# Optimization experiments

Hardware: AMD Instinct MI355X
Metric: run time of the kernel (lower is better)

The kernel has to match this reference:

```python
import jax, jax.numpy as jnp
import numpy as np

D = 1024
M = 32768
B = 4096
TEMP = 1.0
LN_EPS = 1e-5


def setup_inputs() -> dict:
    key = jax.random.key(0)
    ks = jax.random.split(key, 8)
    s = 1.0 / np.sqrt(D)
    return {
        "query": jax.random.normal(ks[0], (B, D), dtype=jnp.float32),
        "mem": jax.random.normal(ks[1], (M, D), dtype=jnp.float32),
        "Wq": jax.random.normal(ks[2], (D, D), dtype=jnp.float32) * s,
        "bq": jax.random.normal(ks[3], (D,), dtype=jnp.float32) * 0.01,
        "Wk": jax.random.normal(ks[4], (D, D), dtype=jnp.float32) * s,
        "bk": jax.random.normal(ks[5], (D,), dtype=jnp.float32) * 0.01,
        "Wv": jax.random.normal(ks[6], (D, D), dtype=jnp.float32) * s,
        "bv": jax.random.normal(ks[7], (D,), dtype=jnp.float32) * 0.01,
        "gamma": jnp.ones((D,), dtype=jnp.float32),
        "beta": jnp.zeros((D,), dtype=jnp.float32),
        "k": 8,
    }


def reference(query, mem, Wq, bq, Wk, bk, Wv, bv, gamma, beta, k):
    d = query.shape[-1]
    # Linear projections (torch Linear: x @ W.T + b)
    q = query @ Wq.T + bq            # [B, d]
    K = mem @ Wk.T + bk              # [M, d]
    V = mem @ Wv.T + bv              # [M, d]
    # Scaled similarity matrix
    sims = (q @ K.T) / (jnp.sqrt(jnp.asarray(d, q.dtype)) * TEMP)  # [B, M]
    # Top-k selection, then irregular gather of V rows
    _, topi = jax.lax.top_k(sims, k)  # [B, k]
    ret = V[topi]                     # [B, k, d]
    # LayerNorm over last dim (elementwise affine, eps=1e-5, biased var)
    mu = jnp.mean(ret, axis=-1, keepdims=True)
    var = jnp.var(ret, axis=-1, keepdims=True)
    return (ret - mu) * jax.lax.rsqrt(var + LN_EPS) * gamma + beta
```

## Files before the change

kernel.cpp:

```cpp
#include <hip/hip_runtime.h>
#include <hip/hip_bf16.h>
#include <math.h>

#define D_DIM 1024
#define B_ROWS 4096
#define M_ROWS 32768
#define TOPK 8
#define TOPC 16
#define TOPB 8
#define NCB (M_ROWS / 128)

typedef __attribute__((ext_vector_type(8))) short bf16x8;
typedef __attribute__((ext_vector_type(4))) float f32x4;

__device__ __forceinline__ unsigned short f32_to_bf16(float f) {
  unsigned int u = __float_as_uint(f);
  unsigned int r = (u + 0x7FFFu + ((u >> 16) & 1u)) >> 16;
  return (unsigned short)r;
}
__device__ __forceinline__ float bf16_to_f32(unsigned short h) {
  return __uint_as_float(((unsigned int)h) << 16);
}
__device__ __forceinline__ void async_copy16(void* lds, const void* g) {
  __builtin_amdgcn_global_load_lds(
      (const __attribute__((address_space(1))) unsigned int*)g,
      (__attribute__((address_space(3))) unsigned int*)lds, 16, 0, 0);
}

template <int N>
__device__ __forceinline__ void insN(float v, int idx,
                                     float* __restrict__ tv,
                                     int* __restrict__ ti) {
  if (v < tv[N - 1]) return;
  if (v == tv[N - 1] && idx > ti[N - 1]) return;
  float cv = v;
  int ci = idx;
#pragma unroll
  for (int p = 0; p < N; ++p) {
    if (cv > tv[p] || (cv == tv[p] && ci < ti[p])) {
      const float t0 = tv[p]; tv[p] = cv; cv = t0;
      const int t1 = ti[p]; ti[p] = ci; ci = t1;
    }
  }
}

__global__ __launch_bounds__(256) void gram_f64(
    const float* __restrict__ Wq, const float* __restrict__ Wk,
    double* __restrict__ G)
{
  __shared__ float sA[2][32][68];
  __shared__ float sB[2][32][68];
  const int tid = threadIdx.x;
  const int tx = tid & 15, ty = tid >> 4;
  const int f0 = blockIdx.x * 64;
  const int e0 = blockIdx.y * 64;

  double acc[4][4];
#pragma unroll
  for (int i = 0; i < 4; ++i)
#pragma unroll
    for (int j = 0; j < 4; ++j) acc[i][j] = 0.0;

  auto STAGE = [&](int d, int k0) {
#pragma unroll
    for (int it = 0; it < 2; ++it) {
      const int L = it * 256 + tid;
      const int kk = L >> 4, c4 = (L & 15) * 4;
      *(float4*)&sA[d][kk][c4] = *(const float4*)(Wq + (size_t)(k0 + kk) * D_DIM + f0 + c4);
      *(float4*)&sB[d][kk][c4] = *(const float4*)(Wk + (size_t)(k0 + kk) * D_DIM + e0 + c4);
    }
  };

  STAGE(0, 0);
  __syncthreads();
  int cur = 0;
  for (int t = 0; t < 32; ++t) {
    if (t < 31) STAGE(cur ^ 1, (t + 1) * 32);
#pragma unroll
    for (int kk = 0; kk < 32; ++kk) {
      const double a[4] = {sA[cur][kk][ty * 4 + 0], sA[cur][kk][ty * 4 + 1],
                           sA[cur][kk][ty * 4 + 2], sA[cur][kk][ty * 4 + 3]};
      const double b[4] = {sB[cur][kk][tx * 4 + 0], sB[cur][kk][tx * 4 + 1],
                           sB[cur][kk][tx * 4 + 2], sB[cur][kk][tx * 4 + 3]};
#pragma unroll
      for (int i = 0; i < 4; ++i)
#pragma unroll
        for (int j = 0; j < 4; ++j)
          acc[i][j] = fma(a[i], b[j], acc[i][j]);
    }
    __syncthreads();
    cur ^= 1;
  }
#pragma unroll
  for (int i = 0; i < 4; ++i)
#pragma unroll
    for (int j = 0; j < 4; ++j)
      G[(size_t)(f0 + ty * 4 + i) * D_DIM + e0 + tx * 4 + j] = acc[i][j];
}

__global__ __launch_bounds__(256) void bias_terms(
    const float* __restrict__ Wq, const float* __restrict__ Wk,
    const float* __restrict__ bq, const float* __restrict__ bk,
    double* __restrict__ wvec, double* __restrict__ ubias,
    double* __restrict__ s0)
{
  const int blk = blockIdx.x;
  const int tid = threadIdx.x;
  if (blk < 4) {
    const int c = blk * 256 + tid;
    double acc = 0.0;
    for (int n = 0; n < D_DIM; ++n)
      acc = fma((double)Wq[(size_t)n * D_DIM + c], (double)bk[n], acc);
    wvec[c] = acc;
  } else if (blk < 8) {
    const int c = (blk - 4) * 256 + tid;
    double acc = 0.0;
    for (int n = 0; n < D_DIM; ++n)
      acc = fma((double)Wk[(size_t)n * D_DIM + c], (double)bq[n], acc);
    ubias[c] = acc;
  } else {
    double acc = 0.0;
#pragma unroll
    for (int i = 0; i < 4; ++i) {
      const int idx = tid * 4 + i;
      acc = fma((double)bq[idx], (double)bk[idx], acc);
    }
#pragma unroll
    for (int off = 32; off > 0; off >>= 1) acc += __shfl_down(acc, off);
    __shared__ double red[4];
    if ((tid & 63) == 0) red[tid >> 6] = acc;
    __syncthreads();
    if (tid == 0) s0[0] = red[0] + red[1] + red[2] + red[3];
  }
}

__global__ __launch_bounds__(256) void qbk_w(
    const float* __restrict__ query, const double* __restrict__ w,
    const double* __restrict__ s0, double* __restrict__ qbk)
{
  const int b = blockIdx.x * 4 + (threadIdx.x >> 6);
  const int lane = threadIdx.x & 63;
  const float* qrow = query + (size_t)b * D_DIM + lane * 16;
  const double* wrow = w + lane * 16;
  double acc = 0.0;
#pragma unroll
  for (int i = 0; i < 16; ++i)
    acc = fma((double)qrow[i], wrow[i], acc);
#pragma unroll
  for (int off = 32; off > 0; off >>= 1) acc += __shfl_down(acc, off);
  if (lane == 0) qbk[b] = acc + s0[0];
}

__global__ __launch_bounds__(256) void uproj_G(
    const float* __restrict__ query, const double* __restrict__ G,
    const double* __restrict__ ubias, double* __restrict__ U)
{
  __shared__ double sAdT[2][32][66];
  __shared__ double sBd[2][32][68];
  const int tid = threadIdx.x;
  const int tx = tid & 15, ty = tid >> 4;
  const int row0 = blockIdx.x * 64;
  const int col0 = blockIdx.y * 64;

  double acc[4][4];
#pragma unroll
  for (int i = 0; i < 4; ++i)
#pragma unroll
    for (int j = 0; j < 4; ++j) acc[i][j] = 0.0;

  auto STAGE = [&](int d, int k0) {
#pragma unroll
    for (int it = 0; it < 2; ++it) {
      const int L = it * 256 + tid;
      const int rowa = L >> 3, c4 = (L & 7) * 4;
      const float4 v =
          *(const float4*)(query + (size_t)(row0 + rowa) * D_DIM + k0 + c4);
      sAdT[d][c4 + 0][rowa] = (double)v.x;
      sAdT[d][c4 + 1][rowa] = (double)v.y;
      sAdT[d][c4 + 2][rowa] = (double)v.z;
      sAdT[d][c4 + 3][rowa] = (double)v.w;
    }
#pragma unroll
    for (int it = 0; it < 4; ++it) {
      const int L = it * 256 + tid;
      const int kk = L >> 5, c2 = (L & 31) * 2;
      *(double2*)&sBd[d][kk][c2] =
          *(const double2*)(G + (size_t)(k0 + kk) * D_DIM + col0 + c2);
    }
  };

  STAGE(0, 0);
  __syncthreads();
  int cur = 0;
  for (int t = 0; t < 32; ++t) {
    if (t < 31) STAGE(cur ^ 1, (t + 1) * 32);
#pragma unroll
    for (int kk = 0; kk < 32; ++kk) {
      const double2 p0 = *(const double2*)&sAdT[cur][kk][ty * 4];
      const double2 p1 = *(const double2*)&sAdT[cur][kk][ty * 4 + 2];
      const double a[4] = {p0.x, p0.y, p1.x, p1.y};
      const double bb[4] = {sBd[cur][kk][tx * 4 + 0], sBd[cur][kk][tx * 4 + 1],
                            sBd[cur][kk][tx * 4 + 2], sBd[cur][kk][tx * 4 + 3]};
#pragma unroll
      for (int i = 0; i < 4; ++i)
#pragma unroll
        for (int j = 0; j < 4; ++j)
          acc[i][j] = fma(a[i], bb[j], acc[i][j]);
    }
    __syncthreads();
    cur ^= 1;
  }
  const double ub[4] = {ubias[col0 + tx * 4 + 0], ubias[col0 + tx * 4 + 1],
                        ubias[col0 + tx * 4 + 2], ubias[col0 + tx * 4 + 3]};
#pragma unroll
  for (int i = 0; i < 4; ++i) {
    const size_t base = (size_t)(row0 + ty * 4 + i) * D_DIM + col0 + tx * 4;
    *(double2*)(U + base)     = (double2){acc[i][0] + ub[0], acc[i][1] + ub[1]};
    *(double2*)(U + base + 2) = (double2){acc[i][2] + ub[2], acc[i][3] + ub[3]};
  }
}

#define SBUF3 12288
__global__ __launch_bounds__(512, 4) void sims_topc_gemm(
    const unsigned short* __restrict__ A, const unsigned short* __restrict__ B,
    float* __restrict__ part_v, int* __restrict__ part_i)
{
  __shared__ unsigned short smem[3 * SBUF3];

  const int tid = threadIdx.x;
  const int lane = tid & 63;
  const int wave = tid >> 6;
  const int wr = wave >> 1;
  const int wc = wave & 1;

  const int bid = blockIdx.x;
  const int x = bid & 7;
  const int t9 = bid >> 3;
  const int cbg = t9 >> 7;
  const int r = (t9 >> 3) & 15;
  const int cbl = t9 & 7;
  const int cb = (x * 4 + cbg) * 8 + cbl;
  const int row0 = r * 256;
  const int col0 = cb * 128;

  const int st_r = lane >> 2;
  const int st_swz = ((lane & 3) ^ ((st_r >> 1) & 3)) * 16;

  auto STAGE = [&](int d, int k0) {
    unsigned short* buf = smem + d * SBUF3;
#pragma unroll
    for (int i = 0; i < 3; ++i) {
      const int seg = wave * 3 + i;
      if (seg < 16) {
        const int grow = row0 + seg * 16 + st_r;
        async_copy16((char*)(buf + seg * 512),
                     (const char*)(A + (size_t)grow * D_DIM + k0) + st_swz);
      } else {
        const int s2 = seg - 16;
        const int grow = col0 + s2 * 16 + st_r;
        async_copy16((char*)(buf + 8192 + s2 * 512),
                     (const char*)(B + (size_t)grow * D_DIM + k0) + st_swz);
      }
    }
  };

  f32x4 acc[4][4];
#pragma unroll
  for (int m = 0; m < 4; ++m)
#pragma unroll
    for (int n = 0; n < 4; ++n) acc[m][n] = (f32x4){0.f, 0.f, 0.f, 0.f};

  auto COMPUTE = [&](int d) {
    const unsigned short* sA = smem + d * SBUF3;
    const unsigned short* sB = sA + 8192;
    bf16x8 af[4], bfr[4];
    const int ch = lane >> 4;
#pragma unroll
    for (int m = 0; m < 4; ++m) {
      const int Ra = wr * 64 + m * 16 + (lane & 15);
      af[m] = *(const bf16x8*)((const char*)sA + Ra * 64 + ((ch ^ ((Ra >> 1) & 3)) * 16));
    }
#pragma unroll
    for (int n = 0; n < 4; ++n) {
      const int Rb = wc * 64 + n * 16 + (lane & 15);
      bfr[n] = *(const bf16x8*)((const char*)sB + Rb * 64 + ((ch ^ ((Rb >> 1) & 3)) * 16));
    }
    __builtin_amdgcn_s_setprio(1);
#pragma unroll
    for (int m = 0; m < 4; ++m)
#pragma unroll
      for (int n = 0; n < 4; ++n)
        acc[m][n] = __builtin_amdgcn_mfma_f32_16x16x32_bf16(af[m], bfr[n], acc[m][n], 0, 0, 0);
    __builtin_amdgcn_s_setprio(0);
  };

  STAGE(0, 0);
  STAGE(1, 32);
  asm volatile("s_waitcnt vmcnt(3)" ::: "memory");
  __builtin_amdgcn_sched_barrier(0);
  __builtin_amdgcn_s_barrier();

  for (int tt = 0; tt < 30; tt += 3) {
    STAGE(2, (tt + 2) * 32);
    COMPUTE(0);
    asm volatile("s_waitcnt vmcnt(3)" ::: "memory");
    __builtin_amdgcn_sched_barrier(0);
    __builtin_amdgcn_s_barrier();

    STAGE(0, (tt + 3) * 32);
    COMPUTE(1);
    asm volatile("s_waitcnt vmcnt(3)" ::: "memory");
    __builtin_amdgcn_sched_barrier(0);
    __builtin_amdgcn_s_barrier();

    STAGE(1, (tt + 4) * 32);
    COMPUTE(2);
    asm volatile("s_waitcnt vmcnt(3)" ::: "memory");
    __builtin_amdgcn_sched_barrier(0);
    __builtin_amdgcn_s_barrier();
  }
  COMPUTE(0);
  asm volatile("s_waitcnt vmcnt(0)" ::: "memory");
  __builtin_amdgcn_sched_barrier(0);
  __builtin_amdgcn_s_barrier();
  COMPUTE(1);
  __builtin_amdgcn_sched_barrier(0);
  __builtin_amdgcn_s_barrier();

#pragma unroll
  for (int m = 0; m < 4; ++m)
#pragma unroll
    for (int n = 0; n < 4; ++n)
#pragma unroll
      for (int rg = 0; rg < 4; ++rg) {
        const int row = wr * 64 + m * 16 + (lane >> 4) * 4 + rg;
        const int colL = wc * 64 + n * 16 + (lane & 15);
        smem[row * 132 + colL] = f32_to_bf16(acc[m][n][rg]);
      }
  __syncthreads();

  {
    const int row = tid & 255;
    const int h = tid >> 8;
    float tv[4];
    int ti_[4];
#pragma unroll
    for (int p = 0; p < 4; ++p) { tv[p] = -INFINITY; ti_[p] = 0; }
    const unsigned short* crow = smem + row * 132 + h * 64;
    const int gcol = col0 + h * 64;
    for (int j = 0; j < 64; j += 4) {
      const ushort4 c4 = *(const ushort4*)(crow + j);
      insN<4>(bf16_to_f32(c4.x), gcol + j + 0, tv, ti_);
      insN<4>(bf16_to_f32(c4.y), gcol + j + 1, tv, ti_);
      insN<4>(bf16_to_f32(c4.z), gcol + j + 2, tv, ti_);
      insN<4>(bf16_to_f32(c4.w), gcol + j + 3, tv, ti_);
    }
    const size_t base = ((size_t)(row0 + row) * NCB + cb) * TOPB + h * 4;
    *(float4*)(part_v + base) = (float4){tv[0], tv[1], tv[2], tv[3]};
    *(int4*)(part_i + base)   = (int4){ti_[0], ti_[1], ti_[2], ti_[3]};
  }
}

__global__ __launch_bounds__(512, 4) void proj256_bf16(
    const unsigned short* __restrict__ A,
    const unsigned short* __restrict__ B,
    const float* __restrict__ bias,
    unsigned short* __restrict__ C)
{
  __shared__ unsigned short smem[3 * SBUF3];

  const int tid = threadIdx.x;
  const int lane = tid & 63;
  const int wave = tid >> 6;
  const int wr = wave >> 1;
  const int wc = wave & 1;

  const int row0 = blockIdx.x * 256;
  const int col0 = blockIdx.y * 128;

  const int st_r = lane >> 2;
  const int st_swz = ((lane & 3) ^ ((st_r >> 1) & 3)) * 16;

  auto STAGE = [&](int d, int k0) {
    unsigned short* buf = smem + d * SBUF3;
#pragma unroll
    for (int i = 0; i < 3; ++i) {
      const int seg = wave * 3 + i;
      if (seg < 16) {
        const int grow = row0 + seg * 16 + st_r;
        async_copy16((char*)(buf + seg * 512),
                     (const char*)(A + (size_t)grow * D_DIM + k0) + st_swz);
      } else {
        const int s2 = seg - 16;
        const int grow = col0 + s2 * 16 + st_r;
        async_copy16((char*)(buf + 8192 + s2 * 512),
                     (const char*)(B + (size_t)grow * D_DIM + k0) + st_swz);
      }
    }
  };

  f32x4 acc[4][4];
#pragma unroll
  for (int m = 0; m < 4; ++m)
#pragma unroll
    for (int n = 0; n < 4; ++n) acc[m][n] = (f32x4){0.f, 0.f, 0.f, 0.f};

  auto COMPUTE = [&](int d) {
    const unsigned short* sA = smem + d * SBUF3;
    const unsigned short* sB = sA + 8192;
    bf16x8 af[4], bfr[4];
    const int ch = lane >> 4;
#pragma unroll
    for (int m = 0; m < 4; ++m) {
      const int Ra = wr * 64 + m * 16 + (lane & 15);
      af[m] = *(const bf16x8*)((const char*)sA + Ra * 64 + ((ch ^ ((Ra >> 1) & 3)) * 16));
    }
#pragma unroll
    for (int n = 0; n < 4; ++n) {
      const int Rb = wc * 64 + n * 16 + (lane & 15);
      bfr[n] = *(const bf16x8*)((const char*)sB + Rb * 64 + ((ch ^ ((Rb >> 1) & 3)) * 16));
    }
    __builtin_amdgcn_s_setprio(1);
#pragma unroll
    for (int m = 0; m < 4; ++m)
#pragma unroll
      for (int n = 0; n < 4; ++n)
        acc[m][n] = __builtin_amdgcn_mfma_f32_16x16x32_bf16(af[m], bfr[n], acc[m][n], 0, 0, 0);
    __builtin_amdgcn_s_setprio(0);
  };

  STAGE(0, 0);
  STAGE(1, 32);
  asm volatile("s_waitcnt vmcnt(3)" ::: "memory");
  __builtin_amdgcn_sched_barrier(0);
  __builtin_amdgcn_s_barrier();

  for (int tt = 0; tt < 30; tt += 3) {
    STAGE(2, (tt + 2) * 32);
    COMPUTE(0);
    asm volatile("s_waitcnt vmcnt(3)" ::: "memory");
    __builtin_amdgcn_sched_barrier(0);
    __builtin_amdgcn_s_barrier();

    STAGE(0, (tt + 3) * 32);
    COMPUTE(1);
    asm volatile("s_waitcnt vmcnt(3)" ::: "memory");
    __builtin_amdgcn_sched_barrier(0);
    __builtin_amdgcn_s_barrier();

    STAGE(1, (tt + 4) * 32);
    COMPUTE(2);
    asm volatile("s_waitcnt vmcnt(3)" ::: "memory");
    __builtin_amdgcn_sched_barrier(0);
    __builtin_amdgcn_s_barrier();
  }
  COMPUTE(0);
  asm volatile("s_waitcnt vmcnt(0)" ::: "memory");
  __builtin_amdgcn_sched_barrier(0);
  __builtin_amdgcn_s_barrier();
  COMPUTE(1);

#pragma unroll
  for (int n = 0; n < 4; ++n) {
    const int col = col0 + wc * 64 + n * 16 + (lane & 15);
    const float bcol = bias[col];
#pragma unroll
    for (int m = 0; m < 4; ++m)
#pragma unroll
      for (int rg = 0; rg < 4; ++rg) {
        const int row = row0 + wr * 64 + m * 16 + (lane >> 4) * 4 + rg;
        C[(size_t)row * D_DIM + col] = f32_to_bf16(acc[m][n][rg] + bcol);
      }
  }
}

__global__ __launch_bounds__(256) void merge_rescore(
    const float* __restrict__ part_v, const int* __restrict__ part_i,
    const double* __restrict__ U, const double* __restrict__ qbk,
    const float* __restrict__ mem, int* __restrict__ topi)
{
  const int r = blockIdx.x;
  const int tid = threadIdx.x;
  const int lane = tid & 63;
  const int wave = tid >> 6;

  float tv[8];
  int ti[8];
  {
    const size_t base = ((size_t)r * NCB + tid) * TOPB;
    const float4 a0 = *(const float4*)(part_v + base);
    const float4 a1 = *(const float4*)(part_v + base + 4);
    const int4 b0 = *(const int4*)(part_i + base);
    const int4 b1 = *(const int4*)(part_i + base + 4);
    tv[0] = a0.x; tv[1] = a0.y; tv[2] = a0.z; tv[3] = a0.w;
    tv[4] = a1.x; tv[5] = a1.y; tv[6] = a1.z; tv[7] = a1.w;
    ti[0] = b0.x; ti[1] = b0.y; ti[2] = b0.z; ti[3] = b0.w;
    ti[4] = b1.x; ti[5] = b1.y; ti[6] = b1.z; ti[7] = b1.w;
  }
  unsigned rem = 0xFFu;

  __shared__ float wv4[4];
  __shared__ int wi4[4];
  __shared__ int winner;
  __shared__ int cand16[TOPC];

  for (int p = 0; p < TOPC; ++p) {
    float bv = -INFINITY;
    int bi = 0x7FFFFFFF;
#pragma unroll
    for (int e = 0; e < 8; ++e) {
      const bool alive = (rem >> e) & 1u;
      const float v = tv[e];
      const int ix = ti[e];
      if (alive && (v > bv || (v == bv && ix < bi))) { bv = v; bi = ix; }
    }
#pragma unroll
    for (int off = 32; off > 0; off >>= 1) {
      const float ov = __shfl_down(bv, off);
      const int oi = __shfl_down(bi, off);
      if (ov > bv || (ov == bv && oi < bi)) { bv = ov; bi = oi; }
    }
    if (lane == 0) { wv4[wave] = bv; wi4[wave] = bi; }
    __syncthreads();
    if (tid == 0) {
      float gv = wv4[0];
      int gi = wi4[0];
#pragma unroll
      for (int w = 1; w < 4; ++w)
        if (wv4[w] > gv || (wv4[w] == gv && wi4[w] < gi)) { gv = wv4[w]; gi = wi4[w]; }
      winner = gi;
      cand16[p] = gi;
    }
    __syncthreads();
    const int wgi = winner;
#pragma unroll
    for (int e = 0; e < 8; ++e)
      if (ti[e] == wgi) rem &= ~(1u << e);
  }

  __shared__ double sval[TOPC];
  __shared__ int sidx[TOPC];

  const double* urow = U + (size_t)r * D_DIM + lane * 16;
  double uv[16];
#pragma unroll
  for (int i = 0; i < 8; ++i) {
    const double2 d2 = *(const double2*)(urow + i * 2);
    uv[i * 2] = d2.x;
    uv[i * 2 + 1] = d2.y;
  }
  const double qb = qbk[r];

  for (int c = wave; c < TOPC; c += 4) {
    const int ci = cand16[c];
    const float* mrow = mem + (size_t)ci * D_DIM + lane * 16;
    double acc = 0.0;
#pragma unroll
    for (int i = 0; i < 4; ++i) {
      const float4 mv = *(const float4*)(mrow + i * 4);
      acc = fma(uv[i * 4 + 0], (double)mv.x, acc);
      acc = fma(uv[i * 4 + 1], (double)mv.y, acc);
      acc = fma(uv[i * 4 + 2], (double)mv.z, acc);
      acc = fma(uv[i * 4 + 3], (double)mv.w, acc);
    }
#pragma unroll
    for (int off = 32; off > 0; off >>= 1) acc += __shfl_down(acc, off);
    if (lane == 0) { sval[c] = acc + qb; sidx[c] = ci; }
  }
  __syncthreads();

  if (tid == 0) {
    bool used[TOPC];
#pragma unroll
    for (int p = 0; p < TOPC; ++p) used[p] = false;
#pragma unroll
    for (int p = 0; p < TOPK; ++p) {
      int best = -1;
      double bv = 0.0;
      int bi = 0;
      for (int c = 0; c < TOPC; ++c) {
        if (used[c]) continue;
        const double v = sval[c];
        const int ix = sidx[c];
        if (best < 0 || v > bv || (v == bv && ix < bi)) { best = c; bv = v; bi = ix; }
      }
      used[best] = true;
      topi[(size_t)r * TOPK + p] = bi;
    }
  }
}

#define N4_MEM   (M_ROWS * D_DIM / 4)
#define N4_QUERY (B_ROWS * D_DIM / 4)
#define N4_W     (D_DIM * D_DIM / 4)
#define N4_TOTAL (N4_MEM + N4_QUERY + 3 * N4_W)

__global__ __launch_bounds__(256) void cast_all_bf16(
    const float* __restrict__ mem, const float* __restrict__ query,
    const float* __restrict__ Wk, const float* __restrict__ Wv,
    const float* __restrict__ Wq,
    unsigned short* __restrict__ membf, unsigned short* __restrict__ querybf,
    unsigned short* __restrict__ wkbf, unsigned short* __restrict__ wvbf,
    unsigned short* __restrict__ wqbf)
{
  int i = blockIdx.x * 256 + threadIdx.x;
  if (i >= N4_TOTAL) return;
  const float* src;
  unsigned short* dst;
  if (i < N4_MEM) { src = mem; dst = membf; }
  else if ((i -= N4_MEM) < N4_QUERY) { src = query; dst = querybf; }
  else if ((i -= N4_QUERY) < N4_W) { src = Wk; dst = wkbf; }
  else if ((i -= N4_W) < N4_W) { src = Wv; dst = wvbf; }
  else { i -= N4_W; src = Wq; dst = wqbf; }
  const float4 v = *(const float4*)(src + (size_t)i * 4);
  ushort4 o;
  o.x = f32_to_bf16(v.x);
  o.y = f32_to_bf16(v.y);
  o.z = f32_to_bf16(v.z);
  o.w = f32_to_bf16(v.w);
  *(ushort4*)(dst + (size_t)i * 4) = o;
}

__global__ __launch_bounds__(256) void gather_ln(
    const unsigned short* __restrict__ V, const int* __restrict__ topi,
    const float* __restrict__ gamma, const float* __restrict__ beta,
    float* __restrict__ out)
{
  const int row = blockIdx.x;
  const int tid = threadIdx.x;
  const int idx = topi[row];
  const unsigned short* src = V + (size_t)idx * D_DIM;
  const ushort4 raw = *(const ushort4*)(src + tid * 4);
  const float v0 = bf16_to_f32(raw.x);
  const float v1 = bf16_to_f32(raw.y);
  const float v2 = bf16_to_f32(raw.z);
  const float v3 = bf16_to_f32(raw.w);
  float s = v0 + v1 + v2 + v3;
  float s2 = v0 * v0 + v1 * v1 + v2 * v2 + v3 * v3;
#pragma unroll
  for (int off = 32; off > 0; off >>= 1) {
    s += __shfl_down(s, off);
    s2 += __shfl_down(s2, off);
  }
  __shared__ float red[8];
  __shared__ float stats[2];
  const int wid = tid >> 6;
  if ((tid & 63) == 0) { red[wid] = s; red[4 + wid] = s2; }
  __syncthreads();
  if (tid == 0) {
    const float S = red[0] + red[1] + red[2] + red[3];
    const float S2 = red[4] + red[5] + red[6] + red[7];
    const float mu = S * (1.0f / D_DIM);
    const float var = S2 * (1.0f / D_DIM) - mu * mu;
    stats[0] = mu;
    stats[1] = rsqrtf(var + 1e-5f);
  }
  __syncthreads();
  const float mu = stats[0], rstd = stats[1];
  const float4 g4 = *(const float4*)(gamma + tid * 4);
  const float4 b4 = *(const float4*)(beta + tid * 4);
  float4 o;
  o.x = (v0 - mu) * rstd * g4.x + b4.x;
  o.y = (v1 - mu) * rstd * g4.y + b4.y;
  o.z = (v2 - mu) * rstd * g4.z + b4.z;
  o.w = (v3 - mu) * rstd * g4.w + b4.w;
  *(float4*)(out + (size_t)row * D_DIM + tid * 4) = o;
}

extern "C" void kernel_launch(void* const* d_in, const int* in_sizes, int n_in,
                              void* d_out, int out_size, void* d_ws, size_t ws_size,
                              hipStream_t stream)
{
  const float* query = (const float*)d_in[0];
  const float* mem   = (const float*)d_in[1];
  const float* Wq    = (const float*)d_in[2];
  const float* bq    = (const float*)d_in[3];
  const float* Wk    = (const float*)d_in[4];
  const float* bk    = (const float*)d_in[5];
  const float* Wv    = (const float*)d_in[6];
  const float* bv    = (const float*)d_in[7];
  const float* gamma = (const float*)d_in[8];
  const float* beta  = (const float*)d_in[9];
  float* out = (float*)d_out;

  char* ws = (char*)d_ws;
  double* u64 = (double*)ws;   ws += (size_t)B_ROWS * D_DIM * sizeof(double);
  double* G = (double*)ws;     ws += (size_t)D_DIM * D_DIM * sizeof(double);
  unsigned short* qbf = (unsigned short*)ws;
  ws += (size_t)B_ROWS * D_DIM * sizeof(unsigned short);
  unsigned short* querybf = (unsigned short*)ws;
  ws += (size_t)B_ROWS * D_DIM * sizeof(unsigned short);
  unsigned short* membf = (unsigned short*)ws;
  ws += (size_t)M_ROWS * D_DIM * sizeof(unsigned short);
  char* Aregion = ws;
  ws += (size_t)M_ROWS * D_DIM * sizeof(unsigned short)
      + 2 * (size_t)B_ROWS * NCB * TOPB * sizeof(float);
  double* wvec = (double*)ws;  ws += (size_t)D_DIM * sizeof(double);
  double* ubias = (double*)ws; ws += (size_t)D_DIM * sizeof(double);
  double* s0 = (double*)ws;    ws += 2 * sizeof(double);
  double* qbk = (double*)ws;   ws += (size_t)B_ROWS * sizeof(double);
  int* topi = (int*)ws;

  unsigned short* Kbf = (unsigned short*)Aregion;
  float* part_v = (float*)(Aregion + (size_t)M_ROWS * D_DIM * sizeof(unsigned short));
  int* part_i = (int*)((char*)part_v + (size_t)B_ROWS * NCB * TOPB * sizeof(float));
  unsigned short* wkbf = (unsigned short*)G;
  unsigned short* wvbf = wkbf + (size_t)D_DIM * D_DIM;
  unsigned short* wqbf = wvbf + (size_t)D_DIM * D_DIM;
  unsigned short* Vbf = (unsigned short*)Aregion;

  gram_f64<<<dim3(16, 16), 256, 0, stream>>>(Wq, Wk, G);
  bias_terms<<<dim3(9), 256, 0, stream>>>(Wq, Wk, bq, bk, wvec, ubias, s0);
  qbk_w<<<dim3(B_ROWS / 4), 256, 0, stream>>>(query, wvec, s0, qbk);
  uproj_G<<<dim3(B_ROWS / 64, D_DIM / 64), 256, 0, stream>>>(query, G, ubias, u64);

  cast_all_bf16<<<dim3((N4_TOTAL + 255) / 256), 256, 0, stream>>>(
      mem, query, Wk, Wv, Wq, membf, querybf, wkbf, wvbf, wqbf);

  proj256_bf16<<<dim3(M_ROWS / 256, D_DIM / 128), 512, 0, stream>>>(membf, wkbf, bk, Kbf);
  proj256_bf16<<<dim3(B_ROWS / 256, D_DIM / 128), 512, 0, stream>>>(querybf, wqbf, bq, qbf);

  sims_topc_gemm<<<dim3((B_ROWS / 256) * NCB), 512, 0, stream>>>(qbf, Kbf, part_v, part_i);
  merge_rescore<<<dim3(B_ROWS), 256, 0, stream>>>(part_v, part_i, u64, qbk, mem, topi);

  proj256_bf16<<<dim3(M_ROWS / 256, D_DIM / 128), 512, 0, stream>>>(membf, wvbf, bv, Vbf);
  gather_ln<<<dim3(B_ROWS * TOPK), 256, 0, stream>>>(Vbf, topi, gamma, beta, out);
}
```

Baseline: 1.154 ms.

## Fuse prep kernels, batch K/Q/V projections, pack top-k partials into u32

Merges the gram, bias, and bf16 cast kernels into one launch. The qbk dot product moves into merge_rescore. The three projection GEMMs become one grid, so K, Q and V are computed together, which needs separate workspace buffers for K and V. Per-tile top-4 partials are packed as bf16 value plus a 16-bit local index in one uint32, halving partial traffic. Partial values are now rounded to bf16, and querybf aliases the parts buffer, which relies on the ordering between kernels.

```diff
diff --git a/kernel.cpp b/kernel.cpp
--- a/kernel.cpp
+++ b/kernel.cpp
@@ -44,81 +44,87 @@
   }
 }
 
-__global__ __launch_bounds__(256) void gram_f64(
+#define N4_MEM   (M_ROWS * D_DIM / 4)
+#define N4_QUERY (B_ROWS * D_DIM / 4)
+#define N4_W     (D_DIM * D_DIM / 4)
+#define N4_TOTAL (N4_MEM + N4_QUERY + 3 * N4_W)
+#define NCAST_BLK ((N4_TOTAL + 255) / 256)
+
+__global__ __launch_bounds__(256) void gram_bias_cast(
     const float* __restrict__ Wq, const float* __restrict__ Wk,
-    double* __restrict__ G)
+    const float* __restrict__ bq, const float* __restrict__ bk,
+    const float* __restrict__ mem, const float* __restrict__ query,
+    const float* __restrict__ Wv,
+    double* __restrict__ G, double* __restrict__ wvec,
+    double* __restrict__ ubias, double* __restrict__ s0,
+    unsigned short* __restrict__ membf, unsigned short* __restrict__ querybf,
+    unsigned short* __restrict__ wkbf, unsigned short* __restrict__ wvbf,
+    unsigned short* __restrict__ wqbf)
 {
   __shared__ float sA[2][32][68];
   __shared__ float sB[2][32][68];
-  const int tid = threadIdx.x;
-  const int tx = tid & 15, ty = tid >> 4;
-  const int f0 = blockIdx.x * 64;
-  const int e0 = blockIdx.y * 64;
-
-  double acc[4][4];
-#pragma unroll
-  for (int i = 0; i < 4; ++i)
-#pragma unroll
-    for (int j = 0; j < 4; ++j) acc[i][j] = 0.0;
-
-  auto STAGE = [&](int d, int k0) {
-#pragma unroll
-    for (int it = 0; it < 2; ++it) {
-      const int L = it * 256 + tid;
-      const int kk = L >> 4, c4 = (L & 15) * 4;
-      *(float4*)&sA[d][kk][c4] = *(const float4*)(Wq + (size_t)(k0 + kk) * D_DIM + f0 + c4);
-      *(float4*)&sB[d][kk][c4] = *(const float4*)(Wk + (size_t)(k0 + kk) * D_DIM + e0 + c4);
-    }
-  };
-
-  STAGE(0, 0);
-  __syncthreads();
-  int cur = 0;
-  for (int t = 0; t < 32; ++t) {
-    if (t < 31) STAGE(cur ^ 1, (t + 1) * 32);
-#pragma unroll
-    for (int kk = 0; kk < 32; ++kk) {
-      const double a[4] = {sA[cur][kk][ty * 4 + 0], sA[cur][kk][ty * 4 + 1],
-                           sA[cur][kk][ty * 4 + 2], sA[cur][kk][ty * 4 + 3]};
-      const double b[4] = {sB[cur][kk][tx * 4 + 0], sB[cur][kk][tx * 4 + 1],
-                           sB[cur][kk][tx * 4 + 2], sB[cur][kk][tx * 4 + 3]};
-#pragma unroll
-      for (int i = 0; i < 4; ++i)
-#pragma unroll
-        for (int j = 0; j < 4; ++j)
-          acc[i][j] = fma(a[i], b[j], acc[i][j]);
-    }
-    __syncthreads();
-    cur ^= 1;
-  }
-#pragma unroll
-  for (int i = 0; i < 4; ++i)
-#pragma unroll
-    for (int j = 0; j < 4; ++j)
-      G[(size_t)(f0 + ty * 4 + i) * D_DIM + e0 + tx * 4 + j] = acc[i][j];
-}
-
-__global__ __launch_bounds__(256) void bias_terms(
-    const float* __restrict__ Wq, const float* __restrict__ Wk,
-    const float* __restrict__ bq, const float* __restrict__ bk,
-    double* __restrict__ wvec, double* __restrict__ ubias,
-    double* __restrict__ s0)
-{
   const int blk = blockIdx.x;
   const int tid = threadIdx.x;
-  if (blk < 4) {
-    const int c = blk * 256 + tid;
+
+  if (blk < 256) {
+    const int tx = tid & 15, ty = tid >> 4;
+    const int f0 = (blk >> 4) * 64;
+    const int e0 = (blk & 15) * 64;
+
+    double acc[4][4];
+#pragma unroll
+    for (int i = 0; i < 4; ++i)
+#pragma unroll
+      for (int j = 0; j < 4; ++j) acc[i][j] = 0.0;
+
+    auto STAGE = [&](int d, int k0) {
+#pragma unroll
+      for (int it = 0; it < 2; ++it) {
+        const int L = it * 256 + tid;
+        const int kk = L >> 4, c4 = (L & 15) * 4;
+        *(float4*)&sA[d][kk][c4] = *(const float4*)(Wq + (size_t)(k0 + kk) * D_DIM + f0 + c4);
+        *(float4*)&sB[d][kk][c4] = *(const float4*)(Wk + (size_t)(k0 + kk) * D_DIM + e0 + c4);
+      }
+    };
+
+    STAGE(0, 0);
+    __syncthreads();
+    int cur = 0;
+    for (int t = 0; t < 32; ++t) {
+      if (t < 31) STAGE(cur ^ 1, (t + 1) * 32);
+#pragma unroll
+      for (int kk = 0; kk < 32; ++kk) {
+        const double a[4] = {sA[cur][kk][ty * 4 + 0], sA[cur][kk][ty * 4 + 1],
+                             sA[cur][kk][ty * 4 + 2], sA[cur][kk][ty * 4 + 3]};
+        const double b[4] = {sB[cur][kk][tx * 4 + 0], sB[cur][kk][tx * 4 + 1],
+                             sB[cur][kk][tx * 4 + 2], sB[cur][kk][tx * 4 + 3]};
+#pragma unroll
+        for (int i = 0; i < 4; ++i)
+#pragma unroll
+          for (int j = 0; j < 4; ++j)
+            acc[i][j] = fma(a[i], b[j], acc[i][j]);
+      }
+      __syncthreads();
+      cur ^= 1;
+    }
+#pragma unroll
+    for (int i = 0; i < 4; ++i)
+#pragma unroll
+      for (int j = 0; j < 4; ++j)
+        G[(size_t)(f0 + ty * 4 + i) * D_DIM + e0 + tx * 4 + j] = acc[i][j];
+  } else if (blk < 260) {
+    const int c = (blk - 256) * 256 + tid;
     double acc = 0.0;
     for (int n = 0; n < D_DIM; ++n)
       acc = fma((double)Wq[(size_t)n * D_DIM + c], (double)bk[n], acc);
     wvec[c] = acc;
-  } else if (blk < 8) {
-    const int c = (blk - 4) * 256 + tid;
+  } else if (blk < 264) {
+    const int c = (blk - 260) * 256 + tid;
     double acc = 0.0;
     for (int n = 0; n < D_DIM; ++n)
       acc = fma((double)Wk[(size_t)n * D_DIM + c], (double)bq[n], acc);
     ubias[c] = acc;
-  } else {
+  } else if (blk == 264) {
     double acc = 0.0;
 #pragma unroll
     for (int i = 0; i < 4; ++i) {
@@ -131,24 +137,24 @@
     if ((tid & 63) == 0) red[tid >> 6] = acc;
     __syncthreads();
     if (tid == 0) s0[0] = red[0] + red[1] + red[2] + red[3];
-  }
-}
-
-__global__ __launch_bounds__(256) void qbk_w(
-    const float* __restrict__ query, const double* __restrict__ w,
-    const double* __restrict__ s0, double* __restrict__ qbk)
-{
-  const int b = blockIdx.x * 4 + (threadIdx.x >> 6);
-  const int lane = threadIdx.x & 63;
-  const float* qrow = query + (size_t)b * D_DIM + lane * 16;
-  const double* wrow = w + lane * 16;
-  double acc = 0.0;
-#pragma unroll
-  for (int i = 0; i < 16; ++i)
-    acc = fma((double)qrow[i], wrow[i], acc);
-#pragma unroll
-  for (int off = 32; off > 0; off >>= 1) acc += __shfl_down(acc, off);
-  if (lane == 0) qbk[b] = acc + s0[0];
+  } else {
+    int i = (blk - 265) * 256 + tid;
+    if (i >= N4_TOTAL) return;
+    const float* src;
+    unsigned short* dst;
+    if (i < N4_MEM) { src = mem; dst = membf; }
+    else if ((i -= N4_MEM) < N4_QUERY) { src = query; dst = querybf; }
+    else if ((i -= N4_QUERY) < N4_W) { src = Wk; dst = wkbf; }
+    else if ((i -= N4_W) < N4_W) { src = Wv; dst = wvbf; }
+    else { i -= N4_W; src = Wq; dst = wqbf; }
+    const float4 v = *(const float4*)(src + (size_t)i * 4);
+    ushort4 o;
+    o.x = f32_to_bf16(v.x);
+    o.y = f32_to_bf16(v.y);
+    o.z = f32_to_bf16(v.z);
+    o.w = f32_to_bf16(v.w);
+    *(ushort4*)(dst + (size_t)i * 4) = o;
+  }
 }
 
 __global__ __launch_bounds__(256) void uproj_G(
@@ -223,7 +229,7 @@
 #define SBUF3 12288
 __global__ __launch_bounds__(512, 4) void sims_topc_gemm(
     const unsigned short* __restrict__ A, const unsigned short* __restrict__ B,
-    float* __restrict__ part_v, int* __restrict__ part_i)
+    unsigned int* __restrict__ parts)
 {
   __shared__ unsigned short smem[3 * SBUF3];
 
@@ -347,25 +353,34 @@
 #pragma unroll
     for (int p = 0; p < 4; ++p) { tv[p] = -INFINITY; ti_[p] = 0; }
     const unsigned short* crow = smem + row * 132 + h * 64;
-    const int gcol = col0 + h * 64;
+    const int lbase = h * 64;
     for (int j = 0; j < 64; j += 4) {
       const ushort4 c4 = *(const ushort4*)(crow + j);
-      insN<4>(bf16_to_f32(c4.x), gcol + j + 0, tv, ti_);
-      insN<4>(bf16_to_f32(c4.y), gcol + j + 1, tv, ti_);
-      insN<4>(bf16_to_f32(c4.z), gcol + j + 2, tv, ti_);
-      insN<4>(bf16_to_f32(c4.w), gcol + j + 3, tv, ti_);
-    }
+      insN<4>(bf16_to_f32(c4.x), lbase + j + 0, tv, ti_);
+      insN<4>(bf16_to_f32(c4.y), lbase + j + 1, tv, ti_);
+      insN<4>(bf16_to_f32(c4.z), lbase + j + 2, tv, ti_);
+      insN<4>(bf16_to_f32(c4.w), lbase + j + 3, tv, ti_);
+    }
+    uint4 pk;
+    pk.x = ((unsigned)f32_to_bf16(tv[0]) << 16) | (unsigned)ti_[0];
+    pk.y = ((unsigned)f32_to_bf16(tv[1]) << 16) | (unsigned)ti_[1];
+    pk.z = ((unsigned)f32_to_bf16(tv[2]) << 16) | (unsigned)ti_[2];
+    pk.w = ((unsigned)f32_to_bf16(tv[3]) << 16) | (unsigned)ti_[3];
     const size_t base = ((size_t)(row0 + row) * NCB + cb) * TOPB + h * 4;
-    *(float4*)(part_v + base) = (float4){tv[0], tv[1], tv[2], tv[3]};
-    *(int4*)(part_i + base)   = (int4){ti_[0], ti_[1], ti_[2], ti_[3]};
-  }
-}
-
-__global__ __launch_bounds__(512, 4) void proj256_bf16(
-    const unsigned short* __restrict__ A,
-    const unsigned short* __restrict__ B,
-    const float* __restrict__ bias,
-    unsigned short* __restrict__ C)
+    *(uint4*)(parts + base) = pk;
+  }
+}
+
+__global__ __launch_bounds__(512, 4) void proj_kqv_bf16(
+    const unsigned short* __restrict__ Amem,
+    const unsigned short* __restrict__ Aquery,
+    const unsigned short* __restrict__ Bk,
+    const unsigned short* __restrict__ Bq,
+    const unsigned short* __restrict__ Bv,
+    const float* __restrict__ bk_, const float* __restrict__ bq_,
+    const float* __restrict__ bv_,
+    unsigned short* __restrict__ Ck, unsigned short* __restrict__ Cq,
+    unsigned short* __restrict__ Cv)
 {
   __shared__ unsigned short smem[3 * SBUF3];
 
@@ -375,7 +390,20 @@
   const int wr = wave >> 1;
   const int wc = wave & 1;
 
-  const int row0 = blockIdx.x * 256;
+  const int bx = blockIdx.x;
+  const unsigned short* A;
+  const unsigned short* B;
+  const float* bias;
+  unsigned short* C;
+  int row0;
+  if (bx < M_ROWS / 256) {
+    A = Amem; B = Bk; bias = bk_; C = Ck; row0 = bx * 256;
+  } else if (bx < M_ROWS / 256 + B_ROWS / 256) {
+    A = Aquery; B = Bq; bias = bq_; C = Cq; row0 = (bx - M_ROWS / 256) * 256;
+  } else {
+    A = Amem; B = Bv; bias = bv_; C = Cv;
+    row0 = (bx - M_ROWS / 256 - B_ROWS / 256) * 256;
+  }
   const int col0 = blockIdx.y * 128;
 
   const int st_r = lane >> 2;
@@ -475,8 +503,9 @@
 }
 
 __global__ __launch_bounds__(256) void merge_rescore(
-    const float* __restrict__ part_v, const int* __restrict__ part_i,
-    const double* __restrict__ U, const double* __restrict__ qbk,
+    const unsigned int* __restrict__ parts,
+    const double* __restrict__ U, const float* __restrict__ query,
+    const double* __restrict__ wvec, const double* __restrict__ s0,
     const float* __restrict__ mem, int* __restrict__ topi)
 {
   const int r = blockIdx.x;
@@ -484,18 +513,37 @@
   const int lane = tid & 63;
   const int wave = tid >> 6;
 
+  __shared__ double qred[4];
+  __shared__ double qbs;
+  {
+    const float* qrow = query + (size_t)r * D_DIM + tid * 4;
+    const double* wrow = wvec + tid * 4;
+    double qa = 0.0;
+#pragma unroll
+    for (int i = 0; i < 4; ++i)
+      qa = fma((double)qrow[i], wrow[i], qa);
+#pragma unroll
+    for (int off = 32; off > 0; off >>= 1) qa += __shfl_down(qa, off);
+    if (lane == 0) qred[wave] = qa;
+    __syncthreads();
+    if (tid == 0) qbs = qred[0] + qred[1] + qred[2] + qred[3] + s0[0];
+  }
+
   float tv[8];
   int ti[8];
   {
     const size_t base = ((size_t)r * NCB + tid) * TOPB;
-    const float4 a0 = *(const float4*)(part_v + base);
-    const float4 a1 = *(const float4*)(part_v + base + 4);
-    const int4 b0 = *(const int4*)(part_i + base);
-    const int4 b1 = *(const int4*)(part_i + base + 4);
-    tv[0] = a0.x; tv[1] = a0.y; tv[2] = a0.z; tv[3] = a0.w;
-    tv[4] = a1.x; tv[5] = a1.y; tv[6] = a1.z; tv[7] = a1.w;
-    ti[0] = b0.x; ti[1] = b0.y; ti[2] = b0.z; ti[3] = b0.w;
-    ti[4] = b1.x; ti[5] = b1.y; ti[6] = b1.z; ti[7] = b1.w;
+    const uint4 w0 = *(const uint4*)(parts + base);
+    const uint4 w1 = *(const uint4*)(parts + base + 4);
+    const int gb = tid * 128;
+    tv[0] = bf16_to_f32((unsigned short)(w0.x >> 16)); ti[0] = gb + (int)(w0.x & 0xFFFFu);
+    tv[1] = bf16_to_f32((unsigned short)(w0.y >> 16)); ti[1] = gb + (int)(w0.y & 0xFFFFu);
+    tv[2] = bf16_to_f32((unsigned short)(w0.z >> 16)); ti[2] = gb + (int)(w0.z & 0xFFFFu);
+    tv[3] = bf16_to_f32((unsigned short)(w0.w >> 16)); ti[3] = gb + (int)(w0.w & 0xFFFFu);
+    tv[4] = bf16_to_f32((unsigned short)(w1.x >> 16)); ti[4] = gb + (int)(w1.x & 0xFFFFu);
+    tv[5] = bf16_to_f32((unsigned short)(w1.y >> 16)); ti[5] = gb + (int)(w1.y & 0xFFFFu);
+    tv[6] = bf16_to_f32((unsigned short)(w1.z >> 16)); ti[6] = gb + (int)(w1.z & 0xFFFFu);
+    tv[7] = bf16_to_f32((unsigned short)(w1.w >> 16)); ti[7] = gb + (int)(w1.w & 0xFFFFu);
   }
   unsigned rem = 0xFFu;
 
@@ -549,7 +597,7 @@
     uv[i * 2] = d2.x;
     uv[i * 2 + 1] = d2.y;
   }
-  const double qb = qbk[r];
+  const double qb = qbs;
 
   for (int c = wave; c < TOPC; c += 4) {
     const int ci = cand16[c];
@@ -588,37 +636,6 @@
       topi[(size_t)r * TOPK + p] = bi;
     }
   }
-}
-
-#define N4_MEM   (M_ROWS * D_DIM / 4)
-#define N4_QUERY (B_ROWS * D_DIM / 4)
-#define N4_W     (D_DIM * D_DIM / 4)
-#define N4_TOTAL (N4_MEM + N4_QUERY + 3 * N4_W)
-
-__global__ __launch_bounds__(256) void cast_all_bf16(
-    const float* __restrict__ mem, const float* __restrict__ query,
-    const float* __restrict__ Wk, const float* __restrict__ Wv,
-    const float* __restrict__ Wq,
-    unsigned short* __restrict__ membf, unsigned short* __restrict__ querybf,
-    unsigned short* __restrict__ wkbf, unsigned short* __restrict__ wvbf,
-    unsigned short* __restrict__ wqbf)
-{
-  int i = blockIdx.x * 256 + threadIdx.x;
-  if (i >= N4_TOTAL) return;
-  const float* src;
-  unsigned short* dst;
-  if (i < N4_MEM) { src = mem; dst = membf; }
-  else if ((i -= N4_MEM) < N4_QUERY) { src = query; dst = querybf; }
-  else if ((i -= N4_QUERY) < N4_W) { src = Wk; dst = wkbf; }
-  else if ((i -= N4_W) < N4_W) { src = Wv; dst = wvbf; }
-  else { i -= N4_W; src = Wq; dst = wqbf; }
-  const float4 v = *(const float4*)(src + (size_t)i * 4);
-  ushort4 o;
-  o.x = f32_to_bf16(v.x);
-  o.y = f32_to_bf16(v.y);
-  o.z = f32_to_bf16(v.z);
-  o.w = f32_to_bf16(v.w);
-  *(ushort4*)(dst + (size_t)i * 4) = o;
 }
 
 __global__ __launch_bounds__(256) void gather_ln(
@@ -688,41 +705,39 @@
   double* G = (double*)ws;     ws += (size_t)D_DIM * D_DIM * sizeof(double);
   unsigned short* qbf = (unsigned short*)ws;
   ws += (size_t)B_ROWS * D_DIM * sizeof(unsigned short);
-  unsigned short* querybf = (unsigned short*)ws;
-  ws += (size_t)B_ROWS * D_DIM * sizeof(unsigned short);
   unsigned short* membf = (unsigned short*)ws;
   ws += (size_t)M_ROWS * D_DIM * sizeof(unsigned short);
-  char* Aregion = ws;
-  ws += (size_t)M_ROWS * D_DIM * sizeof(unsigned short)
-      + 2 * (size_t)B_ROWS * NCB * TOPB * sizeof(float);
+  unsigned short* wkbf = (unsigned short*)ws;
+  ws += (size_t)D_DIM * D_DIM * sizeof(unsigned short);
+  unsigned short* wvbf = (unsigned short*)ws;
+  ws += (size_t)D_DIM * D_DIM * sizeof(unsigned short);
+  unsigned short* wqbf = (unsigned short*)ws;
+  ws += (size_t)D_DIM * D_DIM * sizeof(unsigned short);
+  unsigned short* Kbf = (unsigned short*)ws;
+  ws += (size_t)M_ROWS * D_DIM * sizeof(unsigned short);
+  unsigned short* Vbf = (unsigned short*)ws;
+  ws += (size_t)M_ROWS * D_DIM * sizeof(unsigned short);
+  unsigned int* parts = (unsigned int*)ws;
+  ws += (size_t)B_ROWS * NCB * TOPB * sizeof(unsigned int);
   double* wvec = (double*)ws;  ws += (size_t)D_DIM * sizeof(double);
   double* ubias = (double*)ws; ws += (size_t)D_DIM * sizeof(double);
   double* s0 = (double*)ws;    ws += 2 * sizeof(double);
-  double* qbk = (double*)ws;   ws += (size_t)B_ROWS * sizeof(double);
   int* topi = (int*)ws;
 
-  unsigned short* Kbf = (unsigned short*)Aregion;
-  float* part_v = (float*)(Aregion + (size_t)M_ROWS * D_DIM * sizeof(unsigned short));
-  int* part_i = (int*)((char*)part_v + (size_t)B_ROWS * NCB * TOPB * sizeof(float));
-  unsigned short* wkbf = (unsigned short*)G;
-  unsigned short* wvbf = wkbf + (size_t)D_DIM * D_DIM;
-  unsigned short* wqbf = wvbf + (size_t)D_DIM * D_DIM;
-  unsigned short* Vbf = (unsigned short*)Aregion;
-
-  gram_f64<<<dim3(16, 16), 256, 0, stream>>>(Wq, Wk, G);
-  bias_terms<<<dim3(9), 256, 0, stream>>>(Wq, Wk, bq, bk, wvec, ubias, s0);
-  qbk_w<<<dim3(B_ROWS / 4), 256, 0, stream>>>(query, wvec, s0, qbk);
+  unsigned short* querybf = (unsigned short*)parts;
+
+  gram_bias_cast<<<dim3(265 + NCAST_BLK), 256, 0, stream>>>(
+      Wq, Wk, bq, bk, mem, query, Wv,
+      G, wvec, ubias, s0, membf, querybf, wkbf, wvbf, wqbf);
+
   uproj_G<<<dim3(B_ROWS / 64, D_DIM / 64), 256, 0, stream>>>(query, G, ubias, u64);
 
-  cast_all_bf16<<<dim3((N4_TOTAL + 255) / 256), 256, 0, stream>>>(
-      mem, query, Wk, Wv, Wq, membf, querybf, wkbf, wvbf, wqbf);
-
-  proj256_bf16<<<dim3(M_ROWS / 256, D_DIM / 128), 512, 0, stream>>>(membf, wkbf, bk, Kbf);
-  proj256_bf16<<<dim3(B_ROWS / 256, D_DIM / 128), 512, 0, stream>>>(querybf, wqbf, bq, qbf);
-
-  sims_topc_gemm<<<dim3((B_ROWS / 256) * NCB), 512, 0, stream>>>(qbf, Kbf, part_v, part_i);
-  merge_rescore<<<dim3(B_ROWS), 256, 0, stream>>>(part_v, part_i, u64, qbk, mem, topi);
-
-  proj256_bf16<<<dim3(M_ROWS / 256, D_DIM / 128), 512, 0, stream>>>(membf, wvbf, bv, Vbf);
+  proj_kqv_bf16<<<dim3((2 * M_ROWS + B_ROWS) / 256, D_DIM / 128), 512, 0, stream>>>(
+      membf, querybf, wkbf, wqbf, wvbf, bk, bq, bv, Kbf, qbf, Vbf);
+
+  sims_topc_gemm<<<dim3((B_ROWS / 256) * NCB), 512, 0, stream>>>(qbf, Kbf, parts);
+
+  merge_rescore<<<dim3(B_ROWS), 256, 0, stream>>>(parts, u64, query, wvec, s0, mem, topi);
+
   gather_ln<<<dim3(B_ROWS * TOPK), 256, 0, stream>>>(Vbf, topi, gamma, beta, out);
 }
```

Result: faster. 1.038 ms (-10.1%).
